# Optimization experiments

Hardware: AMD Instinct MI355X
Metric: run time of the kernel (lower is better)

## Reference

```python
import jax, jax.numpy as jnp
import numpy as np

EMBED_DIM = 1024
NUM_HEADS = 16
HEAD_DIM = EMBED_DIM // NUM_HEADS
B, S = 4, 2048


def setup_inputs() -> dict:
    key = jax.random.key(0)
    k_x, k_wqkv, k_bqkv, k_wfc, k_bfc = jax.random.split(key, 5)
    scale = 1.0 / np.sqrt(EMBED_DIM)
    return {
        "x": jax.random.normal(k_x, (B, S, EMBED_DIM), dtype=jnp.float32),
        "w_qkv": jax.random.uniform(k_wqkv, (EMBED_DIM, 3 * EMBED_DIM), jnp.float32, -scale, scale),
        "b_qkv": jax.random.uniform(k_bqkv, (3 * EMBED_DIM,), jnp.float32, -scale, scale),
        "w_fc": jax.random.uniform(k_wfc, (EMBED_DIM, EMBED_DIM), jnp.float32, -scale, scale),
        "b_fc": jax.random.uniform(k_bfc, (EMBED_DIM,), jnp.float32, -scale, scale),
    }


def reference(x, w_qkv, b_qkv, w_fc, b_fc):
    b, s, e = x.shape
    qkv = x @ w_qkv + b_qkv  # [B,S,3E]
    qkv = qkv.reshape(b, s, 3, NUM_HEADS, HEAD_DIM).transpose(2, 0, 3, 1, 4)
    q, k, v = qkv[0], qkv[1], qkv[2]  # each [B,H,S,D]
    attn = jnp.einsum("bhqd,bhkd->bhqk", q, k) / np.sqrt(HEAD_DIM).astype(np.float32)
    attn = jax.nn.softmax(attn, axis=-1)
    out = jnp.einsum("bhqk,bhkd->bhqd", attn, v)  # [B,H,S,D]
    out = out.transpose(0, 2, 1, 3).reshape(b, s, e)
    return out @ w_fc + b_fc
```

## Files before the change

### kernel.cpp

```cpp
#include <hip/hip_runtime.h>
#include <cstdint>

typedef __bf16 bf16;
typedef __bf16 bf16x2 __attribute__((ext_vector_type(2)));
typedef __bf16 bf16x4 __attribute__((ext_vector_type(4)));
typedef __bf16 bf16x8 __attribute__((ext_vector_type(8)));
typedef float  f32x4  __attribute__((ext_vector_type(4)));

#define AS1 __attribute__((address_space(1)))
#define AS3 __attribute__((address_space(3)))

static constexpr int BATCH = 4;
static constexpr int SEQ   = 2048;
static constexpr int EMB   = 1024;
static constexpr int NH    = 16;
static constexpr int HD    = 64;
static constexpr int M     = BATCH * SEQ;

static __device__ __forceinline__ void gload_lds16(const void* g, void* l) {
  __builtin_amdgcn_global_load_lds((AS1 void*)g, (AS3 void*)l, 16, 0, 0);
}

static __device__ __forceinline__ f32x4 mfma16(bf16x8 a, bf16x8 b, f32x4 c) {
  return __builtin_amdgcn_mfma_f32_16x16x32_bf16(a, b, c, 0, 0, 0);
}

static __device__ __forceinline__ float fexp2(float x) {
  float r;
  asm("v_exp_f32 %0, %1" : "=v"(r) : "v"(x));
  return r;
}

__global__ void cast_x_kernel(const float* __restrict__ in, bf16* __restrict__ out) {
  int i = blockIdx.x * 256 + threadIdx.x;
  float4 v = reinterpret_cast<const float4*>(in)[i];
  bf16x4 o;
  o[0] = (bf16)v.x; o[1] = (bf16)v.y; o[2] = (bf16)v.z; o[3] = (bf16)v.w;
  reinterpret_cast<bf16x4*>(out)[i] = o;
}

__global__ void transpose_cast_kernel(const float* __restrict__ w, bf16* __restrict__ wt,
                                      int R, int C) {
  __shared__ float t[32][33];
  int bx = blockIdx.x * 32;
  int by = blockIdx.y * 32;
  int tx = threadIdx.x & 31, ty = threadIdx.x >> 5;
#pragma unroll
  for (int dy = 0; dy < 32; dy += 8)
    t[ty + dy][tx] = w[(long)(by + ty + dy) * C + bx + tx];
  __syncthreads();
#pragma unroll
  for (int dy = 0; dy < 32; dy += 8)
    wt[(long)(bx + ty + dy) * R + by + tx] = (bf16)t[tx][ty + dy];
}

template <int MODE>
__launch_bounds__(256, 2)
__global__ void gemm_kernel(const bf16* __restrict__ A, const bf16* __restrict__ Bt,
                            const float* __restrict__ bias,
                            bf16* __restrict__ qp, bf16* __restrict__ kp,
                            bf16* __restrict__ vp, float* __restrict__ outp) {
  __shared__ bf16 As[128 * 64];
  __shared__ bf16 Bs[128 * 64];
  const int tid = threadIdx.x, lane = tid & 63, wave = tid >> 6;
  const int wr = wave >> 1, wc = wave & 1;
  const int l15 = lane & 15, lg = lane >> 4;

  const int nwgx = gridDim.x;
  const int bidLin = blockIdx.y * nwgx + blockIdx.x;
  const int cpx = (nwgx * gridDim.y) >> 3;
  const int swz = (bidLin & 7) * cpx + (bidLin >> 3);
  const int mBase = (swz / nwgx) * 128, nBase = (swz % nwgx) * 128;

  f32x4 acc[4][4] = {};

  for (int k0 = 0; k0 < 1024; k0 += 64) {
    __syncthreads();
#pragma unroll
    for (int p = 0; p < 4; ++p) {
      int cbase = (p * 4 + wave) * 64;
      int c = cbase + lane;
      int row = c >> 3;
      int gp = (c & 7) ^ (row & 7);
      gload_lds16(&A[(long)(mBase + row) * 1024 + k0 + gp * 8], &As[cbase * 8]);
      gload_lds16(&Bt[(long)(nBase + row) * 1024 + k0 + gp * 8], &Bs[cbase * 8]);
    }
    __syncthreads();

#pragma unroll
    for (int kk = 0; kk < 2; ++kk) {
      bf16x8 af[4], bfp[4];
#pragma unroll
      for (int m = 0; m < 4; ++m) {
        int r = wr * 64 + m * 16 + l15;
        int pg = (kk * 4 + lg) ^ (l15 & 7);
        af[m] = *reinterpret_cast<const bf16x8*>(&As[r * 64 + pg * 8]);
      }
#pragma unroll
      for (int n = 0; n < 4; ++n) {
        int r = wc * 64 + n * 16 + l15;
        int pg = (kk * 4 + lg) ^ (l15 & 7);
        bfp[n] = *reinterpret_cast<const bf16x8*>(&Bs[r * 64 + pg * 8]);
      }
#pragma unroll
      for (int m = 0; m < 4; ++m)
#pragma unroll
        for (int n = 0; n < 4; ++n)
          acc[m][n] = mfma16(af[m], bfp[n], acc[m][n]);
    }
  }

  if constexpr (MODE == 0) {
    __syncthreads();
    auto Es = reinterpret_cast<bf16 (*)[16][72]>(As);
    const int colBase = nBase + wc * 64;
    const int which = colBase >> 10;
    const int hh = (colBase & 1023) >> 6;
    const int rowBase = mBase + wr * 64;
    const int bb = rowBase >> 11;
    const int sBase = rowBase & 2047;
    const long bhOff = (long)(bb * NH + hh);
    const float qscale = (which == 0) ? 0.18033688f : 1.0f;

    float bcol[4];
#pragma unroll
    for (int n = 0; n < 4; ++n) bcol[n] = bias[colBase + n * 16 + l15];

    if (which < 2) {
      bf16* dst = (which == 0 ? qp : kp) + (bhOff * SEQ + sBase) * HD;
#pragma unroll
      for (int m = 0; m < 4; ++m) {
#pragma unroll
        for (int n = 0; n < 4; ++n)
#pragma unroll
          for (int r = 0; r < 4; ++r)
            Es[wave][lg * 4 + r][n * 16 + l15] =
                (bf16)((acc[m][n][r] + bcol[n]) * qscale);
#pragma unroll
        for (int it = 0; it < 2; ++it) {
          int rl = it * 8 + (lane >> 3);
          *reinterpret_cast<bf16x8*>(&dst[(long)(m * 16 + rl) * HD + (lane & 7) * 8]) =
              *reinterpret_cast<const bf16x8*>(&Es[wave][rl][(lane & 7) * 8]);
        }
      }
    } else {
      bf16* dst = vp + (long)bhOff * HD * SEQ + sBase;
#pragma unroll
      for (int n = 0; n < 4; ++n) {
#pragma unroll
        for (int m = 0; m < 4; ++m)
#pragma unroll
          for (int r = 0; r < 4; ++r)
            Es[wave][l15][m * 16 + lg * 4 + r] = (bf16)(acc[m][n][r] + bcol[n]);
#pragma unroll
        for (int it = 0; it < 2; ++it) {
          int rl = it * 8 + (lane >> 3);
          *reinterpret_cast<bf16x8*>(&dst[(long)(n * 16 + rl) * SEQ + (lane & 7) * 8]) =
              *reinterpret_cast<const bf16x8*>(&Es[wave][rl][(lane & 7) * 8]);
        }
      }
    }
  } else {
#pragma unroll
    for (int m = 0; m < 4; ++m) {
#pragma unroll
      for (int n = 0; n < 4; ++n) {
        int col = nBase + wc * 64 + n * 16 + l15;
        float bc = bias[col];
#pragma unroll
        for (int r = 0; r < 4; ++r) {
          int row = mBase + wr * 64 + m * 16 + lg * 4 + r;
          outp[(long)row * 1024 + col] = acc[m][n][r] + bc;
        }
      }
    }
  }
}

__launch_bounds__(256, 4)
__global__ void attn_kernel(const bf16* __restrict__ q, const bf16* __restrict__ k,
                            const bf16* __restrict__ vT, bf16* __restrict__ att) {
  __shared__ __align__(16) char smem[16384];

  const int tid = threadIdx.x, lane = tid & 63, wave = tid >> 6;
  const int l15 = lane & 15, lg = lane >> 4;
  const int orig = (blockIdx.x & 7) * 128 + (blockIdx.x >> 3);
  const int bh = orig >> 4, qt = orig & 15;
  const int b = bh >> 4, h = bh & 15;
  const int qbase = qt * 128 + wave * 32;

  const bf16* Q  = q  + (long)bh * SEQ * HD;
  const bf16* K  = k  + (long)bh * SEQ * HD;
  const bf16* VT = vT + (long)bh * HD * SEQ;

  const int ksrow = wave * 8 + (lane >> 3);
  const int kscol = (lane & 7) ^ (ksrow & 7);
  const int vsrow = wave * 16 + (lane >> 2);
  const int vscol = (lane & 3) ^ ((vsrow >> 1) & 3);

  auto stage = [&](const int c, int kt) {
    gload_lds16(&K[(long)(kt + ksrow) * HD + kscol * 8], smem + c * 4096 + wave * 1024);
    gload_lds16(&VT[(long)vsrow * SEQ + kt + vscol * 8], smem + 8192 + c * 4096 + wave * 1024);
  };
  auto ldK = [&](const int c, int j, int half) -> bf16x8 {
    int row = j * 16 + l15;
    int col = (half * 4 + lg) ^ (row & 7);
    return *reinterpret_cast<const bf16x8*>(smem + c * 4096 + row * 128 + col * 16);
  };
  auto ldVp = [&](const int c, int n) -> bf16x8 {
    int row = n * 16 + l15;
    int sw = (row >> 1) & 3;
    const char* base = smem + 8192 + c * 4096 + row * 64;
    int off0 = (((lg >> 1) ^ sw) * 16) + (lg & 1) * 8;
    int off1 = ((((lg >> 1) + 2) ^ sw) * 16) + (lg & 1) * 8;
    bf16x4 a = *reinterpret_cast<const bf16x4*>(base + off0);
    bf16x4 d = *reinterpret_cast<const bf16x4*>(base + off1);
    bf16x8 r;
    r[0] = a[0]; r[1] = a[1]; r[2] = a[2]; r[3] = a[3];
    r[4] = d[0]; r[5] = d[1]; r[6] = d[2]; r[7] = d[3];
    return r;
  };

  bf16x8 qf[2][2];
#pragma unroll
  for (int g = 0; g < 2; ++g) {
    qf[g][0] = *reinterpret_cast<const bf16x8*>(&Q[(qbase + g * 16 + l15) * HD + lg * 8]);
    qf[g][1] = *reinterpret_cast<const bf16x8*>(&Q[(qbase + g * 16 + l15) * HD + 32 + lg * 8]);
  }

  bf16x8 vones;
#pragma unroll
  for (int i = 0; i < 8; ++i) vones[i] = (bf16)1.0f;

  f32x4 o[2][4] = {};
  f32x4 o4[2] = {};

  auto body = [&](const int c) {
    bf16x8 kf[2][2];
#pragma unroll
    for (int j = 0; j < 2; ++j) {
      kf[j][0] = ldK(c, j, 0);
      kf[j][1] = ldK(c, j, 1);
    }
    bf16x8 vf[4];
#pragma unroll
    for (int n = 0; n < 4; ++n)
      vf[n] = ldVp(c, n);

    f32x4 s[2][2] = {};
    __builtin_amdgcn_s_setprio(1);
#pragma unroll
    for (int g = 0; g < 2; ++g)
#pragma unroll
      for (int j = 0; j < 2; ++j) {
        s[g][j] = mfma16(kf[j][0], qf[g][0], s[g][j]);
        s[g][j] = mfma16(kf[j][1], qf[g][1], s[g][j]);
      }
    __builtin_amdgcn_s_setprio(0);

    bf16x8 pb[2];
#pragma unroll
    for (int g = 0; g < 2; ++g)
#pragma unroll
      for (int r = 0; r < 4; ++r) {
        pb[g][r]     = (bf16)fexp2(s[g][0][r]);
        pb[g][4 + r] = (bf16)fexp2(s[g][1][r]);
      }

    __builtin_amdgcn_s_setprio(1);
#pragma unroll
    for (int g = 0; g < 2; ++g) {
#pragma unroll
      for (int n = 0; n < 4; ++n)
        o[g][n] = mfma16(vf[n], pb[g], o[g][n]);
      o4[g] = mfma16(vones, pb[g], o4[g]);
    }
    __builtin_amdgcn_s_setprio(0);
  };

  stage(0, 0);
  __syncthreads();

  for (int tt = 0; tt < 32; ++tt) {
    const int t0 = tt * 2;
    stage(1, (t0 + 1) * 32);
    body(0);
    __syncthreads();
    if (tt < 31) stage(0, (t0 + 2) * 32);
    body(1);
    __syncthreads();
  }

#pragma unroll
  for (int g = 0; g < 2; ++g) {
    float inv = 1.f / o4[g][0];
    long rowoff = ((long)(b * SEQ + qbase + g * 16 + l15)) * EMB + h * HD;
#pragma unroll
    for (int n = 0; n < 4; ++n) {
      bf16x4 pr;
#pragma unroll
      for (int r = 0; r < 4; ++r) pr[r] = (bf16)(o[g][n][r] * inv);
      *reinterpret_cast<bf16x4*>(&att[rowoff + n * 16 + lg * 4]) = pr;
    }
  }
}

extern "C" void kernel_launch(void* const* d_in, const int* in_sizes, int n_in,
                              void* d_out, int out_size, void* d_ws, size_t ws_size,
                              hipStream_t stream) {
  (void)in_sizes; (void)n_in; (void)out_size; (void)ws_size;
  const float* x     = (const float*)d_in[0];
  const float* w_qkv = (const float*)d_in[1];
  const float* b_qkv = (const float*)d_in[2];
  const float* w_fc  = (const float*)d_in[3];
  const float* b_fc  = (const float*)d_in[4];
  float* out = (float*)d_out;

  uint8_t* ws = (uint8_t*)d_ws;
  const size_t MB = 1024u * 1024u;
  bf16* xb    = (bf16*)(ws + 0 * MB);
  bf16* wqkvT = (bf16*)(ws + 16 * MB);
  bf16* wfcT  = (bf16*)(ws + 22 * MB);
  bf16* qp    = (bf16*)(ws + 24 * MB);
  bf16* kp    = (bf16*)(ws + 40 * MB);
  bf16* vp    = (bf16*)(ws + 56 * MB);
  bf16* att   = xb;

  cast_x_kernel<<<(M * EMB) / 4 / 256, 256, 0, stream>>>(x, xb);
  transpose_cast_kernel<<<dim3(3 * EMB / 32, EMB / 32), 256, 0, stream>>>(w_qkv, wqkvT, EMB, 3 * EMB);
  transpose_cast_kernel<<<dim3(EMB / 32, EMB / 32), 256, 0, stream>>>(w_fc, wfcT, EMB, EMB);

  gemm_kernel<0><<<dim3(3 * EMB / 128, M / 128), 256, 0, stream>>>(
      xb, wqkvT, b_qkv, qp, kp, vp, nullptr);

  attn_kernel<<<1024, 256, 0, stream>>>(qp, kp, vp, att);

  gemm_kernel<1><<<dim3(EMB / 128, M / 128), 256, 0, stream>>>(
      att, wfcT, b_fc, nullptr, nullptr, nullptr, out);
}
```

Measured before the change: 166.0 us.

## Double-buffer LDS tiles in GEMM to overlap global loads with MFMA

The GEMM main loop now uses two LDS buffers for A and B and issues the async global-to-LDS loads for the next K tile before computing on the current one. This is meant to hide global memory latency behind the MFMA work, where before every tile was loaded and then computed in strict sequence. LDS use doubles to 64KB per block, which may limit the two-blocks-per-CU occupancy target. Whether the barrier placement is correct depends on how the compiler inserts vmcnt waits for the LDS loads.

```diff
diff --git a/kernel.cpp b/kernel.cpp
--- a/kernel.cpp
+++ b/kernel.cpp
@@ -60,8 +60,8 @@
                             const float* __restrict__ bias,
                             bf16* __restrict__ qp, bf16* __restrict__ kp,
                             bf16* __restrict__ vp, float* __restrict__ outp) {
-  __shared__ bf16 As[128 * 64];
-  __shared__ bf16 Bs[128 * 64];
+  __shared__ bf16 As[2][128 * 64];
+  __shared__ bf16 Bs[2][128 * 64];
   const int tid = threadIdx.x, lane = tid & 63, wave = tid >> 6;
   const int wr = wave >> 1, wc = wave & 1;
   const int l15 = lane & 15, lg = lane >> 4;
@@ -74,19 +74,18 @@
 
   f32x4 acc[4][4] = {};
 
-  for (int k0 = 0; k0 < 1024; k0 += 64) {
-    __syncthreads();
+  auto stageG = [&](const int c, int k0) {
 #pragma unroll
     for (int p = 0; p < 4; ++p) {
       int cbase = (p * 4 + wave) * 64;
-      int c = cbase + lane;
-      int row = c >> 3;
-      int gp = (c & 7) ^ (row & 7);
-      gload_lds16(&A[(long)(mBase + row) * 1024 + k0 + gp * 8], &As[cbase * 8]);
-      gload_lds16(&Bt[(long)(nBase + row) * 1024 + k0 + gp * 8], &Bs[cbase * 8]);
-    }
-    __syncthreads();
-
+      int cc = cbase + lane;
+      int row = cc >> 3;
+      int gp = (cc & 7) ^ (row & 7);
+      gload_lds16(&A[(long)(mBase + row) * 1024 + k0 + gp * 8], &As[c][cbase * 8]);
+      gload_lds16(&Bt[(long)(nBase + row) * 1024 + k0 + gp * 8], &Bs[c][cbase * 8]);
+    }
+  };
+  auto computeG = [&](const int c) {
 #pragma unroll
     for (int kk = 0; kk < 2; ++kk) {
       bf16x8 af[4], bfp[4];
@@ -94,13 +93,13 @@
       for (int m = 0; m < 4; ++m) {
         int r = wr * 64 + m * 16 + l15;
         int pg = (kk * 4 + lg) ^ (l15 & 7);
-        af[m] = *reinterpret_cast<const bf16x8*>(&As[r * 64 + pg * 8]);
+        af[m] = *reinterpret_cast<const bf16x8*>(&As[c][r * 64 + pg * 8]);
       }
 #pragma unroll
       for (int n = 0; n < 4; ++n) {
         int r = wc * 64 + n * 16 + l15;
         int pg = (kk * 4 + lg) ^ (l15 & 7);
-        bfp[n] = *reinterpret_cast<const bf16x8*>(&Bs[r * 64 + pg * 8]);
+        bfp[n] = *reinterpret_cast<const bf16x8*>(&Bs[c][r * 64 + pg * 8]);
       }
 #pragma unroll
       for (int m = 0; m < 4; ++m)
@@ -108,11 +107,22 @@
         for (int n = 0; n < 4; ++n)
           acc[m][n] = mfma16(af[m], bfp[n], acc[m][n]);
     }
+  };
+
+  stageG(0, 0);
+  __syncthreads();
+  for (int t = 0; t < 8; ++t) {
+    const int k0 = t * 128;
+    stageG(1, k0 + 64);
+    computeG(0);
+    __syncthreads();
+    if (t < 7) stageG(0, k0 + 128);
+    computeG(1);
+    __syncthreads();
   }
 
   if constexpr (MODE == 0) {
-    __syncthreads();
-    auto Es = reinterpret_cast<bf16 (*)[16][72]>(As);
+    auto Es = reinterpret_cast<bf16 (*)[16][72]>(&As[0][0]);
     const int colBase = nBase + wc * 64;
     const int which = colBase >> 10;
     const int hh = (colBase & 1023) >> 6;
```

Measured after the change: 179.7 us. 1.08x slower.
